# Kernel tuning notes

Measured on AMD Instinct MI355X. Metric: run time of the kernel, lower is better.

## Reference

```python
import jax, jax.numpy as jnp
import numpy as np

OUT = 7          # output_size
SR = 2           # sampling_ratio
SCALE = 1.0 / 16.0  # 1 / feature_stride


def _context_boxes(boxes):
    """8 surrounding cells of a 3x3 grid around each RoI; offset-major concat ([8N,4])."""
    x1, y1, x2, y2 = boxes[:, 0], boxes[:, 1], boxes[:, 2], boxes[:, 3]
    w = (x2 - x1) / 3.0
    h = (y2 - y1) / 3.0
    offs = []
    for i in range(3):
        for j in range(3):
            if i == 1 and j == 1:
                continue
            dx = j * w
            dy = i * h
            offs.append(jnp.stack([x1 + dx, y1 + dy, x1 + dx + w, y1 + dy + h], axis=1))
    return jnp.concatenate(offs, axis=0)


def _roi_align_v2(feat, boxes, scale, out, sr):
    """ROIAlignV2 (aligned=True). feat [C,H,W], boxes [B,4] xyxy -> [B,C,out,out]."""
    C, H, W = feat.shape
    # aligned: half-pixel offset, no max(roi_size, 1)
    x1 = boxes[:, 0] * scale - 0.5
    y1 = boxes[:, 1] * scale - 0.5
    bw = (boxes[:, 2] * scale - 0.5 - x1) / out   # bin width
    bh = (boxes[:, 3] * scale - 0.5 - y1) / out   # bin height
    # sample positions along each axis: start + (bin + (s+0.5)/sr) * bin_size  -> [B, out*sr]
    g = jnp.arange(out * sr) // sr
    s = jnp.arange(out * sr) % sr
    t = g + (s + 0.5) / sr                         # [out*sr]
    ys = y1[:, None] + t[None, :] * bh[:, None]    # [B,S]
    xs = x1[:, None] + t[None, :] * bw[:, None]    # [B,S]

    def axis(p, size):
        valid = (p >= -1.0) & (p <= size)
        p = jnp.clip(p, 0.0, size - 1.0)
        lo = jnp.clip(jnp.floor(p), 0.0, size - 2.0).astype(jnp.int32)
        return lo, p - lo, valid

    yl, fy, vy = axis(ys, H)
    xl, fx, vx = axis(xs, W)
    Y = yl[:, :, None]          # [B,S,1]
    X = xl[:, None, :]          # [B,1,S]
    f00 = feat[:, Y, X]         # [C,B,S,S]
    f01 = feat[:, Y, X + 1]
    f10 = feat[:, Y + 1, X]
    f11 = feat[:, Y + 1, X + 1]
    wy = fy[:, :, None]
    wx = fx[:, None, :]
    v = (f00 * (1 - wy) * (1 - wx) + f01 * (1 - wy) * wx
         + f10 * wy * (1 - wx) + f11 * wy * wx)
    v = v * (vy[:, :, None] & vx[:, None, :]).astype(v.dtype)
    # average the sr x sr samples inside each output bin
    B = boxes.shape[0]
    v = v.reshape(C, B, out, sr, out, sr).mean(axis=(3, 5))
    return v.transpose(1, 0, 2, 3)  # [B,C,out,out]


def setup_inputs() -> dict:
    key = jax.random.key(0)
    k1, k2, k3, k4 = jax.random.split(key, 4)
    features = jax.random.normal(k1, (256, 64, 64), dtype=jnp.float32)  # stride-16 map of a 1024px image
    N = 128
    xy = jax.random.uniform(k2, (N, 2), minval=0.0, maxval=800.0)
    wh = jax.random.uniform(k3, (N, 2), minval=32.0, maxval=220.0)
    boxes = jnp.concatenate([xy, xy + wh], axis=1)                      # [N,4] xyxy, image coords
    w_fuse = jax.random.normal(k4, (256, 2048), dtype=jnp.float32) * 0.02  # Conv2d(2048,256,1) weight
    b_fuse = jnp.zeros((256,), dtype=jnp.float32)
    return {"features": features, "boxes": boxes, "w_fuse": w_fuse, "b_fuse": b_fuse}


def reference(features, boxes, w_fuse, b_fuse):
    N = boxes.shape[0]
    cboxes = _context_boxes(boxes)                               # [8N,4] offset-major
    pooled = _roi_align_v2(features, cboxes, SCALE, OUT, SR)     # [8N,256,7,7]
    chunk = pooled.reshape(N, -1, OUT, OUT)                      # faithful to torch .view(N,-1,7,7)
    out = jnp.einsum('nchw,oc->nohw', chunk, w_fuse) + b_fuse[None, :, None, None]
    return jax.nn.relu(out)                                      # [N,256,7,7]
```

## Files before the change

### kernel.cpp

```cpp
#include <hip/hip_runtime.h>
#include <hip/hip_fp16.h>

#define SCALE (1.0f/16.0f)

typedef __attribute__((ext_vector_type(8))) _Float16 f16x8;
typedef __attribute__((ext_vector_type(4))) float f32x4;
typedef __attribute__((ext_vector_type(16))) float f32x16;
typedef __attribute__((ext_vector_type(4))) unsigned int u32x4;
typedef unsigned int u32;

__device__ __forceinline__ void gload16(const void* g, void* l) {
    __builtin_amdgcn_global_load_lds(
        (const __attribute__((address_space(1))) unsigned int*)g,
        (__attribute__((address_space(3))) unsigned int*)l, 16, 0, 0);
}
__device__ __forceinline__ __half2 asH2(u32 v) {
    union { u32 i; __half2 h; } u; u.i = v; return u.h;
}
__device__ __forceinline__ u32 asU32(__half2 h) {
    union { __half2 h; u32 i; } u; u.h = h; return u.i;
}
__device__ __forceinline__ int dupH2(float f) {
    __half h = __float2half_rn(f);
    __half2 d; d.x = h; d.y = h;
    union { __half2 h2; int i; } u; u.h2 = d; return u.i;
}

__global__ void k_prep(const float* __restrict__ feat, __half* __restrict__ featT,
                       const float* __restrict__ wf, __half* __restrict__ wr) {
    __shared__ float t[64][65];
    int b = blockIdx.x;
    if (b < 256) {
        int cb = (b >> 6) << 6;
        int pb = (b & 63) << 6;
        int lx = threadIdx.x & 63, ly = threadIdx.x >> 6;
#pragma unroll
        for (int i = 0; i < 16; ++i) {
            int cl = i*4 + ly;
            t[cl][lx] = feat[(size_t)(cb + cl) * 4096 + pb + lx];
        }
        __syncthreads();
#pragma unroll
        for (int i = 0; i < 16; ++i) {
            int pl = i*4 + ly;
            featT[(size_t)(pb + pl) * 256 + cb + lx] = __float2half_rn(t[lx][pl]);
        }
    } else {
        int ch = (b - 256) * 256 + threadIdx.x;
        int l  = ch & 63;
        int sk = (ch >> 6) & 15;
        int ot = (ch >> 10) & 7;
        int j  = ch >> 13;
        int o = ot*32 + (l & 31);
        int k = j*256 + sk*16 + (l >> 5)*8;
        const float* src = wf + (size_t)o*2048 + k;
        f32x4 a = *(const f32x4*)src;
        f32x4 bb = *(const f32x4*)(src + 4);
        f16x8 p;
#pragma unroll
        for (int u = 0; u < 4; ++u) p[u] = (_Float16)a[u];
#pragma unroll
        for (int u = 0; u < 4; ++u) p[4+u] = (_Float16)bb[u];
        *((f16x8*)wr + ch) = p;
    }
}

__global__ void __launch_bounds__(512) k_fused(
    const __half* __restrict__ featT,
    const float* __restrict__ boxes,
    const __half* __restrict__ wr,
    const float* __restrict__ bfuse,
    float* __restrict__ out)
{
    __shared__ char patch[3][28672];
    __shared__ char Pl[2][16384];
    __shared__ int4 tabs[4][2][7];
    __shared__ int  pbs[4][2];
    __shared__ float bx_lds[32];

    int tid = threadIdx.x;
    int lane = tid & 63, wid = tid >> 6;
    int r31 = lane & 31, l5 = lane >> 5;
    int bid = blockIdx.x;
    int n  = bid & 127;
    int hh = bid >> 7;
    int hw0 = hh * 25;
    int HWn = hh ? 24 : 25;
    bool producer = wid < 4;

    int nb_base = (n & 15) * 8;
    int off = n >> 4;
    int t3 = off + (off >= 4 ? 1 : 0);
    int ci = t3 / 3, cj = t3 - ci*3;

    if (tid < 32) bx_lds[tid] = boxes[nb_base*4 + tid];
    {
        int padrows = 32 - HWn;
        for (int i = tid; i < padrows*32*2; i += 512) {
            int b = i / (padrows*32);
            int rem = i - b*(padrows*32);
            int row = HWn + (rem >> 5), slot = rem & 31;
            *(u32x4*)(Pl[b] + row*512 + slot*16) = (u32x4){0,0,0,0};
        }
    }

    auto tablesW = [&](int jj) {
        if (wid < 2) {
            int isy = wid;
            float bx1 = bx_lds[jj*4+0], by1 = bx_lds[jj*4+1];
            float bx2 = bx_lds[jj*4+2], by2 = bx_lds[jj*4+3];
            float w3 = (bx2-bx1)*(1.f/3.f), h3 = (by2-by1)*(1.f/3.f);
            float org  = isy ? (by1 + ci*h3)*SCALE - 0.5f : (bx1 + cj*w3)*SCALE - 0.5f;
            float step = (isy ? h3 : w3) * (SCALE*(1.f/14.f));
            float sc = isy ? 0.25f : 1.f;
            float p = org + ((float)lane + 0.5f)*step;
            float pc = fminf(fmaxf(p, 0.f), 63.f);
            float fl = fminf(floorf(pc), 62.f);
            float fr = pc - fl;
            float c0 = __shfl(fl, 2*lane);
            float c1 = __shfl(fl, 2*lane+1);
            float f  = __shfl(fr, 2*lane);
            float f2 = __shfl(fr, 2*lane+1);
            float fl0 = __shfl(fl, 0);
            int base = min((int)fl0, 56);
            float d = c1 - c0;
            float a0 = sc*((1.f-f) + (1.f-d)*(1.f-f2));
            float a1 = sc*(f + (1.f-d)*f2 + d*(1.f-f2));
            float a2 = sc*(d*f2);
            if (lane < 7) {
                int4 e;
                e.x = (int)c0 - base;
                e.y = dupH2(a0); e.z = dupH2(a1); e.w = dupH2(a2);
                tabs[jj & 3][isy][lane] = e;
            }
            if (lane == 0) pbs[jj & 3][isy] = base;
        }
    };

    auto stage = [&](int jj) {
        int xb = pbs[jj & 3][0], yb = pbs[jj & 3][1];
        char* pd = patch[jj % 3];
#pragma unroll
        for (int i = 0; i < 7; ++i) {
            int seg = wid + 4*i;
            int row = seg >> 2, q = seg & 3;
            const __half* src = featT + ((size_t)((yb + row)*64 + xb))*256 + q*512 + lane*8;
            gload16(src, pd + row*4096 + q*1024);
        }
    };

    auto pool = [&](int jj) {
        int buf = jj & 1;
        int co = tid & 31;
        int e0 = tid >> 5;
        const char* pb = patch[jj % 3] + co*16;
#pragma unroll
        for (int it = 0; it < 4; ++it) {
            if (it*8 < HWn) {
                int e = e0 + it*8;
                bool on = e < HWn;
                int ec = on ? e : 0;
                int g = hw0 + ec;
                int h = (g*37) >> 8, w = g - h*7;
                int4 tx = tabs[jj & 3][0][w], ty = tabs[jj & 3][1][h];
                int px0 = tx.x, py0 = ty.x;
                int lx2 = min(px0 + 2, 7), ly2 = min(py0 + 2, 6);
                const char* r0 = pb + (py0*8 + px0)*512;
                const char* r1 = pb + (min(py0+1,6)*8 + px0)*512;
                const char* r2 = pb + (ly2*8 + px0)*512;
                int dx2 = (lx2 - px0)*512;
                u32x4 F00 = *(const u32x4*)(r0);
                u32x4 F01 = *(const u32x4*)(r0 + 512);
                u32x4 F02 = *(const u32x4*)(r0 + dx2);
                u32x4 F10 = *(const u32x4*)(r1);
                u32x4 F11 = *(const u32x4*)(r1 + 512);
                u32x4 F12 = *(const u32x4*)(r1 + dx2);
                u32x4 F20 = *(const u32x4*)(r2);
                u32x4 F21 = *(const u32x4*)(r2 + 512);
                u32x4 F22 = *(const u32x4*)(r2 + dx2);
                __half2 xa = asH2(tx.y), xb2 = asH2(tx.z), xc = asH2(tx.w);
                __half2 ya = asH2(ty.y), yb2 = asH2(ty.z), yc = asH2(ty.w);
                u32x4 res;
#pragma unroll
                for (int s = 0; s < 4; ++s) {
                    __half2 q0 = __hfma2(asH2(F02[s]), xc, __hfma2(asH2(F01[s]), xb2, __hmul2(asH2(F00[s]), xa)));
                    __half2 q1 = __hfma2(asH2(F12[s]), xc, __hfma2(asH2(F11[s]), xb2, __hmul2(asH2(F10[s]), xa)));
                    __half2 q2 = __hfma2(asH2(F22[s]), xc, __hfma2(asH2(F21[s]), xb2, __hmul2(asH2(F20[s]), xa)));
                    res[s] = asU32(__hfma2(q2, yc, __hfma2(q1, yb2, __hmul2(q0, ya))));
                }
                if (on)
                    *(u32x4*)(Pl[buf] + ec*512 + ((co*16) ^ ((ec & 31) << 4))) = res;
            }
        }
    };

    int cw = wid - 4;
    u32x4 Wf[32];
    f32x16 acc0, acc1;
#pragma unroll
    for (int i = 0; i < 16; ++i) { acc0[i] = 0.f; acc1[i] = 0.f; }

    auto prefW_half = [&](int j, int sb) {
#pragma unroll
        for (int t = 0; t < 2; ++t) {
            int otg = cw*2 + t;
            const u32x4* wb = (const u32x4*)wr + ((size_t)((j*8 + otg)*16))*64 + lane;
#pragma unroll
            for (int s = 0; s < 8; ++s) Wf[t*16 + sb*8 + s] = wb[(sb*8 + s)*64];
        }
    };

    auto gemm_half = [&](int j, int sb) {
        const char* plb = (j & 1) ? Pl[1] : Pl[0];
#pragma unroll
        for (int s = 0; s < 8; ++s) {
            int sk = sb*8 + s;
            int byo = r31*512 + ((sk*32 + l5*16) ^ (r31 << 4));
            f16x8 pf = *(const f16x8*)(plb + byo);
            acc0 = __builtin_amdgcn_mfma_f32_32x32x16_f16(
                __builtin_bit_cast(f16x8, Wf[sk]), pf, acc0, 0, 0, 0);
            acc1 = __builtin_amdgcn_mfma_f32_32x32x16_f16(
                __builtin_bit_cast(f16x8, Wf[16 + sk]), pf, acc1, 0, 0, 0);
        }
    };

    __syncthreads();
    tablesW(0); tablesW(1); tablesW(2); tablesW(3);
    __syncthreads();
    if (producer) {
        stage(0); stage(1); stage(2);
        asm volatile("s_waitcnt vmcnt(14)" ::: "memory");
        __builtin_amdgcn_sched_barrier(0);
        pool(0);
        asm volatile("s_waitcnt lgkmcnt(0)" ::: "memory");
    } else {
        prefW_half(0, 0); prefW_half(0, 1);
    }
    __builtin_amdgcn_s_barrier();
    __builtin_amdgcn_sched_barrier(0);

#pragma unroll
    for (int j = 0; j < 8; ++j) {
        if (producer) {
            if (j < 5) stage(j+3);
            if (j < 7) {
                if (j < 5)       asm volatile("s_waitcnt vmcnt(14)" ::: "memory");
                else if (j == 5) asm volatile("s_waitcnt vmcnt(7)"  ::: "memory");
                else             asm volatile("s_waitcnt vmcnt(0)"  ::: "memory");
                __builtin_amdgcn_sched_barrier(0);
                pool(j+1);
            }
            if (j < 4) tablesW(j+4);
            asm volatile("s_waitcnt lgkmcnt(0)" ::: "memory");
        } else {
            gemm_half(j, 0);
            if (j < 7) prefW_half(j+1, 0);
            gemm_half(j, 1);
            if (j < 7) prefW_half(j+1, 1);
            asm volatile("s_waitcnt lgkmcnt(0)" ::: "memory");
        }
        __builtin_amdgcn_s_barrier();
        __builtin_amdgcn_sched_barrier(0);
    }

    if (!producer) {
        int hw = hw0 + r31;
        bool ok = r31 < HWn;
        float* ob = out + (size_t)n*12544 + hw;
#pragma unroll
        for (int t = 0; t < 2; ++t) {
            f32x16 a = t ? acc1 : acc0;
            int otb = (cw*2 + t)*32;
#pragma unroll
            for (int reg = 0; reg < 16; ++reg) {
                int o = otb + (reg & 3) + 8*(reg >> 2) + 4*l5;
                float v = a[reg] + bfuse[o];
                if (ok) ob[(size_t)o*49] = fmaxf(v, 0.f);
            }
        }
    }
}

extern "C" void kernel_launch(void* const* d_in, const int* in_sizes, int n_in,
                              void* d_out, int out_size, void* d_ws, size_t ws_size,
                              hipStream_t stream) {
    const float* feat  = (const float*)d_in[0];
    const float* boxes = (const float*)d_in[1];
    const float* wf    = (const float*)d_in[2];
    const float* bfuse = (const float*)d_in[3];
    float* out = (float*)d_out;

    char* ws = (char*)d_ws;
    __half* wr    = (__half*)ws;
    __half* featT = (__half*)(ws + (1u<<20));

    k_prep<<<512, 256, 0, stream>>>(feat, featT, wf, wr);
    k_fused<<<256, 512, 0, stream>>>(featT, boxes, wr, bfuse, out);
}
```

Baseline: 29.41 us.

## Split fused kernel over K halves instead of spatial halves, add reduction kernel

The 256 blocks are now split along the reduction dimension (4 of 8 context offsets per block) rather than along the 49 output positions. Each block pools only 4 patches and computes all 49 positions with four MFMA accumulators per wave, so each block loads half the weights and does half the pooling work. The old split made both blocks redundantly pool every patch. Partial sums go to a workspace buffer, and a new elementwise kernel adds the two halves, applies bias and ReLU. The cost is an extra launch and a 12.8 MB round trip of partial results through memory.

```diff
diff --git a/kernel.cpp b/kernel.cpp
--- a/kernel.cpp
+++ b/kernel.cpp
@@ -69,23 +69,20 @@
     const __half* __restrict__ featT,
     const float* __restrict__ boxes,
     const __half* __restrict__ wr,
-    const float* __restrict__ bfuse,
-    float* __restrict__ out)
+    float* __restrict__ part)
 {
-    __shared__ char patch[3][28672];
-    __shared__ char Pl[2][16384];
+    __shared__ char patch[2][28672];
+    __shared__ char Pl[2][32768];
     __shared__ int4 tabs[4][2][7];
     __shared__ int  pbs[4][2];
-    __shared__ float bx_lds[32];
+    __shared__ float bx_lds[16];
 
     int tid = threadIdx.x;
     int lane = tid & 63, wid = tid >> 6;
     int r31 = lane & 31, l5 = lane >> 5;
     int bid = blockIdx.x;
     int n  = bid & 127;
-    int hh = bid >> 7;
-    int hw0 = hh * 25;
-    int HWn = hh ? 24 : 25;
+    int kh = bid >> 7;
     bool producer = wid < 4;
 
     int nb_base = (n & 15) * 8;
@@ -93,15 +90,12 @@
     int t3 = off + (off >= 4 ? 1 : 0);
     int ci = t3 / 3, cj = t3 - ci*3;
 
-    if (tid < 32) bx_lds[tid] = boxes[nb_base*4 + tid];
-    {
-        int padrows = 32 - HWn;
-        for (int i = tid; i < padrows*32*2; i += 512) {
-            int b = i / (padrows*32);
-            int rem = i - b*(padrows*32);
-            int row = HWn + (rem >> 5), slot = rem & 31;
-            *(u32x4*)(Pl[b] + row*512 + slot*16) = (u32x4){0,0,0,0};
-        }
+    if (tid < 16) bx_lds[tid] = boxes[(nb_base + kh*4)*4 + tid];
+    for (int i = tid; i < 15*32*2; i += 512) {
+        int b = i / (15*32);
+        int rem = i - b*(15*32);
+        int row = 49 + (rem >> 5), slot = rem & 31;
+        *(u32x4*)(Pl[b] + row*512 + slot*16) = (u32x4){0,0,0,0};
     }
 
     auto tablesW = [&](int jj) {
@@ -131,15 +125,15 @@
                 int4 e;
                 e.x = (int)c0 - base;
                 e.y = dupH2(a0); e.z = dupH2(a1); e.w = dupH2(a2);
-                tabs[jj & 3][isy][lane] = e;
+                tabs[jj][isy][lane] = e;
             }
-            if (lane == 0) pbs[jj & 3][isy] = base;
+            if (lane == 0) pbs[jj][isy] = base;
         }
     };
 
     auto stage = [&](int jj) {
-        int xb = pbs[jj & 3][0], yb = pbs[jj & 3][1];
-        char* pd = patch[jj % 3];
+        int xb = pbs[jj][0], yb = pbs[jj][1];
+        char* pd = patch[jj & 1];
 #pragma unroll
         for (int i = 0; i < 7; ++i) {
             int seg = wid + 4*i;
@@ -153,58 +147,56 @@
         int buf = jj & 1;
         int co = tid & 31;
         int e0 = tid >> 5;
-        const char* pb = patch[jj % 3] + co*16;
-#pragma unroll
-        for (int it = 0; it < 4; ++it) {
-            if (it*8 < HWn) {
-                int e = e0 + it*8;
-                bool on = e < HWn;
-                int ec = on ? e : 0;
-                int g = hw0 + ec;
-                int h = (g*37) >> 8, w = g - h*7;
-                int4 tx = tabs[jj & 3][0][w], ty = tabs[jj & 3][1][h];
-                int px0 = tx.x, py0 = ty.x;
-                int lx2 = min(px0 + 2, 7), ly2 = min(py0 + 2, 6);
-                const char* r0 = pb + (py0*8 + px0)*512;
-                const char* r1 = pb + (min(py0+1,6)*8 + px0)*512;
-                const char* r2 = pb + (ly2*8 + px0)*512;
-                int dx2 = (lx2 - px0)*512;
-                u32x4 F00 = *(const u32x4*)(r0);
-                u32x4 F01 = *(const u32x4*)(r0 + 512);
-                u32x4 F02 = *(const u32x4*)(r0 + dx2);
-                u32x4 F10 = *(const u32x4*)(r1);
-                u32x4 F11 = *(const u32x4*)(r1 + 512);
-                u32x4 F12 = *(const u32x4*)(r1 + dx2);
-                u32x4 F20 = *(const u32x4*)(r2);
-                u32x4 F21 = *(const u32x4*)(r2 + 512);
-                u32x4 F22 = *(const u32x4*)(r2 + dx2);
-                __half2 xa = asH2(tx.y), xb2 = asH2(tx.z), xc = asH2(tx.w);
-                __half2 ya = asH2(ty.y), yb2 = asH2(ty.z), yc = asH2(ty.w);
-                u32x4 res;
-#pragma unroll
-                for (int s = 0; s < 4; ++s) {
-                    __half2 q0 = __hfma2(asH2(F02[s]), xc, __hfma2(asH2(F01[s]), xb2, __hmul2(asH2(F00[s]), xa)));
-                    __half2 q1 = __hfma2(asH2(F12[s]), xc, __hfma2(asH2(F11[s]), xb2, __hmul2(asH2(F10[s]), xa)));
-                    __half2 q2 = __hfma2(asH2(F22[s]), xc, __hfma2(asH2(F21[s]), xb2, __hmul2(asH2(F20[s]), xa)));
-                    res[s] = asU32(__hfma2(q2, yc, __hfma2(q1, yb2, __hmul2(q0, ya))));
-                }
-                if (on)
-                    *(u32x4*)(Pl[buf] + ec*512 + ((co*16) ^ ((ec & 31) << 4))) = res;
+        const char* pb = patch[jj & 1] + co*16;
+#pragma unroll
+        for (int it = 0; it < 7; ++it) {
+            int e = e0 + it*8;
+            bool on = e < 49;
+            int ec = on ? e : 0;
+            int h = (ec*37) >> 8, w = ec - h*7;
+            int4 tx = tabs[jj][0][w], ty = tabs[jj][1][h];
+            int px0 = tx.x, py0 = ty.x;
+            int lx2 = min(px0 + 2, 7), ly2 = min(py0 + 2, 6);
+            const char* r0 = pb + (py0*8 + px0)*512;
+            const char* r1 = pb + (min(py0+1,6)*8 + px0)*512;
+            const char* r2 = pb + (ly2*8 + px0)*512;
+            int dx2 = (lx2 - px0)*512;
+            u32x4 F00 = *(const u32x4*)(r0);
+            u32x4 F01 = *(const u32x4*)(r0 + 512);
+            u32x4 F02 = *(const u32x4*)(r0 + dx2);
+            u32x4 F10 = *(const u32x4*)(r1);
+            u32x4 F11 = *(const u32x4*)(r1 + 512);
+            u32x4 F12 = *(const u32x4*)(r1 + dx2);
+            u32x4 F20 = *(const u32x4*)(r2);
+            u32x4 F21 = *(const u32x4*)(r2 + 512);
+            u32x4 F22 = *(const u32x4*)(r2 + dx2);
+            __half2 xa = asH2(tx.y), xb2 = asH2(tx.z), xc = asH2(tx.w);
+            __half2 ya = asH2(ty.y), yb2 = asH2(ty.z), yc = asH2(ty.w);
+            u32x4 res;
+#pragma unroll
+            for (int s = 0; s < 4; ++s) {
+                __half2 q0 = __hfma2(asH2(F02[s]), xc, __hfma2(asH2(F01[s]), xb2, __hmul2(asH2(F00[s]), xa)));
+                __half2 q1 = __hfma2(asH2(F12[s]), xc, __hfma2(asH2(F11[s]), xb2, __hmul2(asH2(F10[s]), xa)));
+                __half2 q2 = __hfma2(asH2(F22[s]), xc, __hfma2(asH2(F21[s]), xb2, __hmul2(asH2(F20[s]), xa)));
+                res[s] = asU32(__hfma2(q2, yc, __hfma2(q1, yb2, __hmul2(q0, ya))));
             }
+            if (on)
+                *(u32x4*)(Pl[buf] + ec*512 + ((co*16) ^ ((ec & 31) << 4))) = res;
         }
     };
 
     int cw = wid - 4;
     u32x4 Wf[32];
-    f32x16 acc0, acc1;
-#pragma unroll
-    for (int i = 0; i < 16; ++i) { acc0[i] = 0.f; acc1[i] = 0.f; }
+    f32x16 accA0, accA1, accB0, accB1;
+#pragma unroll
+    for (int i = 0; i < 16; ++i) { accA0[i]=0.f; accA1[i]=0.f; accB0[i]=0.f; accB1[i]=0.f; }
 
     auto prefW_half = [&](int j, int sb) {
+        int jg = kh*4 + j;
 #pragma unroll
         for (int t = 0; t < 2; ++t) {
             int otg = cw*2 + t;
-            const u32x4* wb = (const u32x4*)wr + ((size_t)((j*8 + otg)*16))*64 + lane;
+            const u32x4* wb = (const u32x4*)wr + ((size_t)((jg*8 + otg)*16))*64 + lane;
 #pragma unroll
             for (int s = 0; s < 8; ++s) Wf[t*16 + sb*8 + s] = wb[(sb*8 + s)*64];
         }
@@ -215,12 +207,18 @@
 #pragma unroll
         for (int s = 0; s < 8; ++s) {
             int sk = sb*8 + s;
-            int byo = r31*512 + ((sk*32 + l5*16) ^ (r31 << 4));
-            f16x8 pf = *(const f16x8*)(plb + byo);
-            acc0 = __builtin_amdgcn_mfma_f32_32x32x16_f16(
-                __builtin_bit_cast(f16x8, Wf[sk]), pf, acc0, 0, 0, 0);
-            acc1 = __builtin_amdgcn_mfma_f32_32x32x16_f16(
-                __builtin_bit_cast(f16x8, Wf[16 + sk]), pf, acc1, 0, 0, 0);
+            int by0 = r31*512 + ((sk*32 + l5*16) ^ (r31 << 4));
+            int by1 = (32 + r31)*512 + ((sk*32 + l5*16) ^ (r31 << 4));
+            f16x8 pf0 = *(const f16x8*)(plb + by0);
+            f16x8 pf1 = *(const f16x8*)(plb + by1);
+            accA0 = __builtin_amdgcn_mfma_f32_32x32x16_f16(
+                __builtin_bit_cast(f16x8, Wf[sk]), pf0, accA0, 0, 0, 0);
+            accA1 = __builtin_amdgcn_mfma_f32_32x32x16_f16(
+                __builtin_bit_cast(f16x8, Wf[sk]), pf1, accA1, 0, 0, 0);
+            accB0 = __builtin_amdgcn_mfma_f32_32x32x16_f16(
+                __builtin_bit_cast(f16x8, Wf[16 + sk]), pf0, accB0, 0, 0, 0);
+            accB1 = __builtin_amdgcn_mfma_f32_32x32x16_f16(
+                __builtin_bit_cast(f16x8, Wf[16 + sk]), pf1, accB1, 0, 0, 0);
         }
     };
 
@@ -228,8 +226,8 @@
     tablesW(0); tablesW(1); tablesW(2); tablesW(3);
     __syncthreads();
     if (producer) {
-        stage(0); stage(1); stage(2);
-        asm volatile("s_waitcnt vmcnt(14)" ::: "memory");
+        stage(0); stage(1);
+        asm volatile("s_waitcnt vmcnt(7)" ::: "memory");
         __builtin_amdgcn_sched_barrier(0);
         pool(0);
         asm volatile("s_waitcnt lgkmcnt(0)" ::: "memory");
@@ -240,23 +238,22 @@
     __builtin_amdgcn_sched_barrier(0);
 
 #pragma unroll
-    for (int j = 0; j < 8; ++j) {
+    for (int j = 0; j < 4; ++j) {
         if (producer) {
-            if (j < 5) stage(j+3);
-            if (j < 7) {
-                if (j < 5)       asm volatile("s_waitcnt vmcnt(14)" ::: "memory");
-                else if (j == 5) asm volatile("s_waitcnt vmcnt(7)"  ::: "memory");
-                else             asm volatile("s_waitcnt vmcnt(0)"  ::: "memory");
+            if (j == 0) stage(2);
+            else if (j == 1) stage(3);
+            if (j < 3) {
+                if (j < 2) asm volatile("s_waitcnt vmcnt(7)" ::: "memory");
+                else       asm volatile("s_waitcnt vmcnt(0)" ::: "memory");
                 __builtin_amdgcn_sched_barrier(0);
                 pool(j+1);
             }
-            if (j < 4) tablesW(j+4);
             asm volatile("s_waitcnt lgkmcnt(0)" ::: "memory");
         } else {
             gemm_half(j, 0);
-            if (j < 7) prefW_half(j+1, 0);
+            if (j < 3) prefW_half(j+1, 0);
             gemm_half(j, 1);
-            if (j < 7) prefW_half(j+1, 1);
+            if (j < 3) prefW_half(j+1, 1);
             asm volatile("s_waitcnt lgkmcnt(0)" ::: "memory");
         }
         __builtin_amdgcn_s_barrier();
@@ -264,21 +261,38 @@
     }
 
     if (!producer) {
-        int hw = hw0 + r31;
-        bool ok = r31 < HWn;
-        float* ob = out + (size_t)n*12544 + hw;
+        float* pb = part + ((size_t)(kh*128 + n)) * 12544;
 #pragma unroll
         for (int t = 0; t < 2; ++t) {
-            f32x16 a = t ? acc1 : acc0;
-            int otb = (cw*2 + t)*32;
-#pragma unroll
-            for (int reg = 0; reg < 16; ++reg) {
-                int o = otb + (reg & 3) + 8*(reg >> 2) + 4*l5;
-                float v = a[reg] + bfuse[o];
-                if (ok) ob[(size_t)o*49] = fmaxf(v, 0.f);
+#pragma unroll
+            for (int hwt = 0; hwt < 2; ++hwt) {
+                f32x16 a = t ? (hwt ? accB1 : accB0) : (hwt ? accA1 : accA0);
+                int hw = hwt*32 + r31;
+                bool ok = hw < 49;
+                int otb = (cw*2 + t)*32;
+#pragma unroll
+                for (int reg = 0; reg < 16; ++reg) {
+                    int o = otb + (reg & 3) + 8*(reg >> 2) + 4*l5;
+                    if (ok) pb[(size_t)o*49 + hw] = a[reg];
+                }
             }
         }
     }
+}
+
+__global__ void k_reduce(const float* __restrict__ part, const float* __restrict__ bfuse,
+                         float* __restrict__ out) {
+    int i4 = blockIdx.x * 256 + threadIdx.x;
+    f32x4 a = ((const f32x4*)part)[i4];
+    f32x4 b = ((const f32x4*)(part + 1605632))[i4];
+    int base = i4 * 4;
+    f32x4 r;
+#pragma unroll
+    for (int u = 0; u < 4; ++u) {
+        int o = ((base + u) / 49) & 255;
+        r[u] = fmaxf(a[u] + b[u] + bfuse[o], 0.f);
+    }
+    ((f32x4*)out)[i4] = r;
 }
 
 extern "C" void kernel_launch(void* const* d_in, const int* in_sizes, int n_in,
@@ -293,7 +307,9 @@
     char* ws = (char*)d_ws;
     __half* wr    = (__half*)ws;
     __half* featT = (__half*)(ws + (1u<<20));
+    float*  part  = (float*)(ws + (4u<<20));
 
     k_prep<<<512, 256, 0, stream>>>(feat, featT, wf, wr);
-    k_fused<<<256, 512, 0, stream>>>(featT, boxes, wr, bfuse, out);
-}
+    k_fused<<<256, 512, 0, stream>>>(featT, boxes, wr, part);
+    k_reduce<<<1568, 256, 0, stream>>>(part, bfuse, out);
+}
```

Measured after the change: 41.66 us. 1.42x slower.
